# Kernel optimization log

Hardware: AMD Instinct MI355X
Metric: run time of the kernel (lower is better)

The kernel has to match this reference:

```python
import jax, jax.numpy as jnp
import numpy as np

D_MODEL = 1024
NHEAD = 16
HEAD_DIM = D_MODEL // NHEAD
D_FF = 4096
EPS = 1e-8


def rmsnorm(x, w):
    # matches torch: norm = ||x||_2 / sqrt(d); out = w * x / (rms + eps)
    rms = jnp.linalg.norm(x, axis=-1, keepdims=True) / np.sqrt(x.shape[-1])
    return w * (x / (rms + EPS))


def setup_inputs() -> dict:
    key = jax.random.key(0)
    ks = jax.random.split(key, 11)
    B, S = 4, 2048
    init = lambda k, shape, fan_in: jax.random.uniform(k, shape, jnp.float32, -1.0, 1.0) / np.sqrt(fan_in)
    return {
        "src": jax.random.normal(ks[0], (B, S, D_MODEL), jnp.float32),
        "qkv_w": init(ks[1], (D_MODEL, 3 * D_MODEL), D_MODEL),
        "qkv_b": init(ks[2], (3 * D_MODEL,), D_MODEL),
        "out_w": init(ks[3], (D_MODEL, D_MODEL), D_MODEL),
        "out_b": init(ks[4], (D_MODEL,), D_MODEL),
        "ff1_w": init(ks[5], (D_MODEL, D_FF), D_MODEL),
        "ff1_b": init(ks[6], (D_FF,), D_MODEL),
        "ff2_w": init(ks[7], (D_FF, D_MODEL), D_FF),
        "ff2_b": init(ks[8], (D_MODEL,), D_FF),
        "norm1_w": jnp.ones((D_MODEL,), jnp.float32),
        "norm2_w": jnp.ones((D_MODEL,), jnp.float32),
    }


def reference(src, qkv_w, qkv_b, out_w, out_b, ff1_w, ff1_b, ff2_w, ff2_b, norm1_w, norm2_w):
    B, S, _ = src.shape
    # --- pre-norm attention block ---
    x = rmsnorm(src, norm1_w)
    qkv = x @ qkv_w + qkv_b                     # [B,S,3*D]
    qkv = qkv.reshape(B, S, 3, NHEAD, HEAD_DIM)
    q, k, v = qkv[:, :, 0], qkv[:, :, 1], qkv[:, :, 2]   # [B,S,H,D]
    scores = jnp.einsum('bshd,bthd->bhst', q, k) / np.sqrt(HEAD_DIM)
    attn = jax.nn.softmax(scores, axis=-1)
    ctx = jnp.einsum('bhst,bthd->bshd', attn, v).reshape(B, S, D_MODEL)
    src = src + ctx @ out_w + out_b
    # --- pre-norm FFN block ---
    y = rmsnorm(src, norm2_w)
    h = jax.nn.gelu(y @ ff1_w + ff1_b, approximate=False)
    src = src + h @ ff2_w + ff2_b
    return src
```

## Files before the change

### kernel.cpp

```cpp
#include <hip/hip_runtime.h>
#include <hip/hip_bf16.h>

#define DM   1024
#define DFF  4096
#define NH   16
#define HD   64
#define SEQ  2048
#define BATCH 4
#define NTOK (BATCH*SEQ)

typedef float  f32x4  __attribute__((ext_vector_type(4)));
typedef short  bf16x8 __attribute__((ext_vector_type(8)));

#define SBAR() asm volatile("s_barrier" ::: "memory")
#define S_VMCNT(N) asm volatile("s_waitcnt vmcnt(" #N ")" ::: "memory")

__device__ __forceinline__ unsigned short f2bf(float f) {
    unsigned int x = __builtin_bit_cast(unsigned int, f);
    x += 0x7fff + ((x >> 16) & 1);
    return (unsigned short)(x >> 16);
}
__device__ __forceinline__ float bf2f(unsigned short u) {
    unsigned int x = (unsigned int)u << 16;
    return __builtin_bit_cast(float, x);
}

__device__ __forceinline__ float fexp2(float x) {
    float r; asm("v_exp_f32 %0, %1" : "=v"(r) : "v"(x)); return r;
}
__device__ __forceinline__ float frcp(float x) {
    float r; asm("v_rcp_f32 %0, %1" : "=v"(r) : "v"(x)); return r;
}

__device__ __forceinline__ void gload_lds16(const void* g, void* l) {
    __builtin_amdgcn_global_load_lds(
        (const __attribute__((address_space(1))) unsigned int*)g,
        (__attribute__((address_space(3))) unsigned int*)l,
        16, 0, 0);
}

__device__ __forceinline__ int swz(int row, int elem) { return elem ^ ((row & 7) << 3); }

__global__ __launch_bounds__(256)
void prep_all(const float* __restrict__ qkv_w, const float* __restrict__ out_w,
              const float* __restrict__ ff1_w, const float* __restrict__ ff2_w,
              unsigned short* __restrict__ qkv_wt, unsigned short* __restrict__ out_wt,
              unsigned short* __restrict__ ff1_wt, unsigned short* __restrict__ ff2_wt,
              const float* __restrict__ src, const float* __restrict__ n1_w,
              unsigned short* __restrict__ xb)
{
    __shared__ float tile[32][33];
    int b = blockIdx.x;
    if (b < 12288) {
        const float* W; unsigned short* Wt; int K, N, bx, by;
        if (b < 3072)      { W = qkv_w; Wt = qkv_wt; K = 1024; N = 3072; bx = b % 96;  by = b / 96;  }
        else if (b < 4096) { int i = b - 3072; W = out_w; Wt = out_wt; K = 1024; N = 1024; bx = i % 32;  by = i / 32; }
        else if (b < 8192) { int i = b - 4096; W = ff1_w; Wt = ff1_wt; K = 1024; N = 4096; bx = i % 128; by = i / 128; }
        else               { int i = b - 8192; W = ff2_w; Wt = ff2_wt; K = 4096; N = 1024; bx = i % 32;  by = i / 32; }
        int n0 = bx * 32, k0 = by * 32;
        int tx = threadIdx.x & 31, ty = threadIdx.x >> 5;
        #pragma unroll
        for (int i = 0; i < 4; ++i)
            tile[ty + i*8][tx] = W[(size_t)(k0 + ty + i*8) * N + n0 + tx];
        __syncthreads();
        #pragma unroll
        for (int i = 0; i < 4; ++i)
            Wt[(size_t)(n0 + ty + i*8) * K + k0 + tx] = f2bf(tile[tx][ty + i*8]);
    } else {
        int row = b - 12288, t = threadIdx.x;
        float4 v = ((const float4*)(src + (size_t)row * DM))[t];
        float ss = v.x*v.x + v.y*v.y + v.z*v.z + v.w*v.w;
        #pragma unroll
        for (int m = 1; m < 64; m <<= 1) ss += __shfl_xor(ss, m);
        if ((t & 63) == 0) tile[0][t >> 6] = ss;
        __syncthreads();
        float tot = tile[0][0] + tile[0][1] + tile[0][2] + tile[0][3];
        float rms = sqrtf(tot) * (1.f / 32.f);
        float inv = 1.f / (rms + 1e-8f);
        float4 wv = ((const float4*)n1_w)[t];
        unsigned int lo = (unsigned int)f2bf(v.x*inv*wv.x) | ((unsigned int)f2bf(v.y*inv*wv.y) << 16);
        unsigned int hi = (unsigned int)f2bf(v.z*inv*wv.z) | ((unsigned int)f2bf(v.w*inv*wv.w) << 16);
        uint2 pk; pk.x = lo; pk.y = hi;
        *(uint2*)(xb + (size_t)row * DM + t * 4) = pk;
    }
}

__global__ __launch_bounds__(256)
void rmsnorm_kernel(const unsigned short* __restrict__ inp, const float* __restrict__ w,
                    unsigned short* __restrict__ out)
{
    __shared__ float red[4];
    int row = blockIdx.x, t = threadIdx.x;
    ushort4 u = ((const ushort4*)(inp + (size_t)row * DM))[t];
    float x0 = bf2f(u.x), x1 = bf2f(u.y), x2 = bf2f(u.z), x3 = bf2f(u.w);
    float ss = x0*x0 + x1*x1 + x2*x2 + x3*x3;
    #pragma unroll
    for (int m = 1; m < 64; m <<= 1) ss += __shfl_xor(ss, m);
    if ((t & 63) == 0) red[t >> 6] = ss;
    __syncthreads();
    float tot = red[0] + red[1] + red[2] + red[3];
    float rms = sqrtf(tot) * (1.f / 32.f);
    float inv = 1.f / (rms + 1e-8f);
    float4 wv = ((const float4*)w)[t];
    unsigned int lo = (unsigned int)f2bf(x0*inv*wv.x) | ((unsigned int)f2bf(x1*inv*wv.y) << 16);
    unsigned int hi = (unsigned int)f2bf(x2*inv*wv.z) | ((unsigned int)f2bf(x3*inv*wv.w) << 16);
    uint2 pk; pk.x = lo; pk.y = hi;
    *(uint2*)(out + (size_t)row * DM + t * 4) = pk;
}

template<int MODE, int NB>
__global__ __launch_bounds__(512, 2)
void gemm_tpl(const unsigned short* __restrict__ A,
              const unsigned short* __restrict__ Bt,
              const float* __restrict__ bias,
              int N, int K, int nx,
              const float* __restrict__ residf,
              const unsigned short* __restrict__ residb,
              float* __restrict__ outf,
              unsigned short* __restrict__ outb,
              unsigned short* __restrict__ q,
              unsigned short* __restrict__ kk,
              unsigned short* __restrict__ vt)
{
    constexpr int NJ = NB / 64;
    constexpr int WN = NB / 4;
    __shared__ __align__(16) unsigned short Atile[2][2][256 * 32];
    __shared__ __align__(16) unsigned short Btile[2][2][NB * 32];
    const int tid = threadIdx.x, w = tid >> 6, l = tid & 63;
    const int lr = l & 15, lh = l >> 4;
    const int wm = w >> 2, wn = w & 3;
    const int nwg = gridDim.x, cpx = nwg >> 3;
    const int sid = (blockIdx.x & 7) * cpx + (blockIdx.x >> 3);
    const int by = sid / nx, bx = sid - by * nx;
    const int m0 = by * 256, n0 = bx * NB;
    const int nkt = K >> 6;
    const int srow = w * 16 + (l >> 2);
    const int scol = (((l & 3) ^ (srow & 3)) << 3);

    auto stageA = [&](int kt, int ks, int half, int bi) {
        int r0 = half * 128;
        gload_lds16(A + (size_t)(m0 + r0 + srow) * K + kt * 64 + ks * 32 + scol,
                    &Atile[bi][ks][(r0 + w * 16) * 32]);
    };
    auto stageB = [&](int kt, int ks, int half, int bi) {
        int r0 = half * 128;
        gload_lds16(Bt + (size_t)(n0 + r0 + srow) * K + kt * 64 + ks * 32 + scol,
                    &Btile[bi][ks][(r0 + w * 16) * 32]);
    };

    f32x4 acc[8][NJ];
    #pragma unroll
    for (int a = 0; a < 8; ++a)
        #pragma unroll
        for (int j = 0; j < NJ; ++j) acc[a][j] = {0.f, 0.f, 0.f, 0.f};

    #pragma unroll
    for (int ks = 0; ks < 2; ++ks) {
        stageA(0, ks, 0, 0); stageA(0, ks, 1, 0);
        stageB(0, ks, 0, 0);
        if (NB == 256) stageB(0, ks, 1, 0);
    }

    int bi = 0;
    for (int t = 0; t < nkt; ++t) {
        #pragma unroll
        for (int ks = 0; ks < 2; ++ks) {
            if (ks == 0 || t + 1 < nkt) {
                if constexpr (NB == 256) { S_VMCNT(4); } else { S_VMCNT(3); }
            } else {
                S_VMCNT(0);
            }
            SBAR();
            bf16x8 bB[NJ];
            #pragma unroll
            for (int j = 0; j < NJ; ++j) {
                int row = wn * WN + j * 16 + lr;
                bB[j] = *(const bf16x8*)&Btile[bi][ks][row * 32 + ((lh ^ (row & 3)) << 3)];
            }
            #pragma unroll
            for (int rho = 0; rho < 2; ++rho) {
                bf16x8 aA[4];
                #pragma unroll
                for (int i = 0; i < 4; ++i) {
                    int row = wm * 128 + rho * 64 + i * 16 + lr;
                    aA[i] = *(const bf16x8*)&Atile[bi][ks][row * 32 + ((lh ^ (row & 3)) << 3)];
                }
                if (t + 1 < nkt) {
                    if (rho == 0) { stageA(t + 1, ks, 0, bi ^ 1); stageA(t + 1, ks, 1, bi ^ 1); }
                    else          { stageB(t + 1, ks, 0, bi ^ 1);
                                    if (NB == 256) stageB(t + 1, ks, 1, bi ^ 1); }
                }
                SBAR();
                __builtin_amdgcn_s_setprio(1);
                #pragma unroll
                for (int i = 0; i < 4; ++i)
                    #pragma unroll
                    for (int j = 0; j < NJ; ++j)
                        acc[rho * 4 + i][j] = __builtin_amdgcn_mfma_f32_16x16x32_bf16(
                            aA[i], bB[j], acc[rho * 4 + i][j], 0, 0, 0);
                __builtin_amdgcn_s_setprio(0);
            }
        }
        bi ^= 1;
    }

    #pragma unroll
    for (int a = 0; a < 8; ++a) {
        const int rho = a >> 2, i = a & 3;
        #pragma unroll
        for (int j = 0; j < NJ; ++j) {
            const int col = n0 + wn * WN + j * 16 + lr;
            const int row0 = m0 + wm * 128 + rho * 64 + i * 16 + lh * 4;
            if (MODE == 0) {
                float v0 = acc[a][j][0] + bias[col];
                float v1 = acc[a][j][1] + bias[col];
                float v2 = acc[a][j][2] + bias[col];
                float v3 = acc[a][j][3] + bias[col];
                int wh = col >> 10, h = (col >> 6) & 15, d = col & 63;
                int b = row0 >> 11, s0 = row0 & 2047;
                size_t base = (size_t)(b * NH + h);
                if (wh == 0) {
                    q[(base * SEQ + s0    ) * HD + d] = f2bf(v0 * 0.18033688f);
                    q[(base * SEQ + s0 + 1) * HD + d] = f2bf(v1 * 0.18033688f);
                    q[(base * SEQ + s0 + 2) * HD + d] = f2bf(v2 * 0.18033688f);
                    q[(base * SEQ + s0 + 3) * HD + d] = f2bf(v3 * 0.18033688f);
                } else if (wh == 1) {
                    kk[(base * SEQ + s0    ) * HD + d] = f2bf(v0);
                    kk[(base * SEQ + s0 + 1) * HD + d] = f2bf(v1);
                    kk[(base * SEQ + s0 + 2) * HD + d] = f2bf(v2);
                    kk[(base * SEQ + s0 + 3) * HD + d] = f2bf(v3);
                } else {
                    uint2 pk;
                    pk.x = (unsigned int)f2bf(v0) | ((unsigned int)f2bf(v1) << 16);
                    pk.y = (unsigned int)f2bf(v2) | ((unsigned int)f2bf(v3) << 16);
                    *(uint2*)&vt[(base * HD + d) * SEQ + s0] = pk;
                }
            } else {
                #pragma unroll
                for (int r = 0; r < 4; ++r) {
                    int row = row0 + r;
                    float v = acc[a][j][r] + bias[col];
                    if (MODE == 2) {
                        float x = v;
                        float t2 = fmaf(x * x * x, 0.044715f, x);
                        float av = fminf(t2 * 2.3022079f, 80.f);
                        float u = fexp2(av);
                        float g = x * u * frcp(u + 1.f);
                        outb[(size_t)row * N + col] = f2bf(g);
                    } else if (MODE == 3) {
                        outf[(size_t)row * N + col] = v + bf2f(residb[(size_t)row * N + col]);
                    } else {
                        outb[(size_t)row * N + col] = f2bf(v + residf[(size_t)row * N + col]);
                    }
                }
            }
        }
    }
}

__global__ __launch_bounds__(256, 2)
void attn_kernel(const unsigned short* __restrict__ q,
                 const unsigned short* __restrict__ k,
                 const unsigned short* __restrict__ vt,
                 unsigned short* __restrict__ ctx)
{
    __shared__ __align__(16) unsigned short Ks[2][64 * 64];
    __shared__ __align__(16) unsigned short Vs[2][64 * 64];
    __shared__ __align__(16) unsigned short PQ[4][64 * 64];

    const int tid = threadIdx.x, w = tid >> 6, l = tid & 63;
    const int lr = l & 15, lh = l >> 4;

    const int sid = (blockIdx.x & 7) * 64 + (blockIdx.x >> 3);
    const int bh = sid >> 3, qt = sid & 7;
    const int b = bh >> 4, h = bh & 15;

    const int rloc = l >> 3;
    const int cswz = (((l & 7) ^ rloc) << 3);

    const unsigned short* kbase0 = k  + (size_t)bh * SEQ * HD;
    const unsigned short* vbase0 = vt + (size_t)bh * HD * SEQ;
    const int NT = SEQ / 64;

    auto stageK = [&](int t, int buf) {
        const unsigned short* kb = kbase0 + (size_t)t * 64 * HD;
        #pragma unroll
        for (int c = 0; c < 2; ++c) {
            int r0 = (w * 2 + c) * 8;
            gload_lds16(kb + (size_t)(r0 + rloc) * HD + cswz, &Ks[buf][r0 * 64]);
        }
    };
    auto stageV = [&](int t, int buf) {
        const unsigned short* vb = vbase0 + t * 64;
        #pragma unroll
        for (int c = 0; c < 2; ++c) {
            int d0 = w * 16 + c * 8;
            gload_lds16(vb + (size_t)(d0 + rloc) * SEQ + cswz, &Vs[buf][d0 * 64]);
        }
    };

    unsigned short* Pw = &PQ[w][0];
    const unsigned short* qbase = q + ((size_t)bh * SEQ + qt * 256 + w * 64) * HD;
    #pragma unroll
    for (int c = 0; c < 8; ++c) {
        int r0 = c * 8;
        gload_lds16(qbase + (size_t)(r0 + rloc) * HD + cswz, &Pw[r0 * 64]);
    }
    stageK(0, 0);
    stageV(0, 0);
    S_VMCNT(4);
    bf16x8 aq[4][2];
    #pragma unroll
    for (int g = 0; g < 4; ++g) {
        int row = g * 16 + lr;
        aq[g][0] = *(const bf16x8*)&Pw[row * 64 + swz(row,      lh * 8)];
        aq[g][1] = *(const bf16x8*)&Pw[row * 64 + swz(row, 32 + lh * 8)];
    }
    __syncthreads();

    bf16x8 vone;
    #pragma unroll
    for (int i = 0; i < 8; ++i) vone[i] = (short)0x3F80;

    f32x4 lacc[4];
    f32x4 o[4][4];
    #pragma unroll
    for (int g = 0; g < 4; ++g) {
        lacc[g] = {0.f, 0.f, 0.f, 0.f};
        #pragma unroll
        for (int nf = 0; nf < 4; ++nf) o[g][nf] = {0.f, 0.f, 0.f, 0.f};
    }

    for (int t = 0; t < NT; ++t) {
        const int cur = t & 1;
        if (t + 1 < NT) { stageK(t + 1, cur ^ 1); stageV(t + 1, cur ^ 1); }

        const unsigned short* Kc = &Ks[cur][0];
        const unsigned short* Vc = &Vs[cur][0];

        bf16x8 kb[4][2];
        #pragma unroll
        for (int j = 0; j < 4; ++j) {
            int kr = j * 16 + lr;
            kb[j][0] = *(const bf16x8*)&Kc[kr * 64 + swz(kr,      lh * 8)];
            kb[j][1] = *(const bf16x8*)&Kc[kr * 64 + swz(kr, 32 + lh * 8)];
        }

        #pragma unroll
        for (int g = 0; g < 4; ++g) {
            f32x4 sc[4];
            __builtin_amdgcn_s_setprio(1);
            #pragma unroll
            for (int j = 0; j < 4; ++j) {
                f32x4 z = {0.f, 0.f, 0.f, 0.f};
                z = __builtin_amdgcn_mfma_f32_16x16x32_bf16(kb[j][0], aq[g][0], z, 0, 0, 0);
                z = __builtin_amdgcn_mfma_f32_16x16x32_bf16(kb[j][1], aq[g][1], z, 0, 0, 0);
                sc[j] = z;
            }
            __builtin_amdgcn_s_setprio(0);

            int prow = g * 16 + lr;
            #pragma unroll
            for (int j = 0; j < 4; ++j) {
                float p0 = fexp2(sc[j][0]), p1 = fexp2(sc[j][1]);
                float p2 = fexp2(sc[j][2]), p3 = fexp2(sc[j][3]);
                unsigned int w0, w1;
                asm("v_cvt_pk_bf16_f32 %0, %1, %2" : "=v"(w0) : "v"(p0), "v"(p1));
                asm("v_cvt_pk_bf16_f32 %0, %1, %2" : "=v"(w1) : "v"(p2), "v"(p3));
                int k0 = j * 16 + lh * 4;
                int e = prow * 64 + (k0 ^ ((prow & 7) << 3));
                uint2 pk; pk.x = w0; pk.y = w1;
                *(uint2*)&Pw[e] = pk;
            }
        }

        bf16x8 ap[4][2];
        #pragma unroll
        for (int g = 0; g < 4; ++g) {
            int prow = g * 16 + lr;
            ap[g][0] = *(const bf16x8*)&Pw[prow * 64 + swz(prow,      lh * 8)];
            ap[g][1] = *(const bf16x8*)&Pw[prow * 64 + swz(prow, 32 + lh * 8)];
        }
        __builtin_amdgcn_s_setprio(1);
        #pragma unroll
        for (int g = 0; g < 4; ++g) {
            lacc[g] = __builtin_amdgcn_mfma_f32_16x16x32_bf16(ap[g][0], vone, lacc[g], 0, 0, 0);
            lacc[g] = __builtin_amdgcn_mfma_f32_16x16x32_bf16(ap[g][1], vone, lacc[g], 0, 0, 0);
        }
        #pragma unroll
        for (int nf = 0; nf < 4; ++nf) {
            int vr = nf * 16 + lr;
            bf16x8 vb0 = *(const bf16x8*)&Vc[vr * 64 + swz(vr,      lh * 8)];
            bf16x8 vb1 = *(const bf16x8*)&Vc[vr * 64 + swz(vr, 32 + lh * 8)];
            #pragma unroll
            for (int g = 0; g < 4; ++g) {
                o[g][nf] = __builtin_amdgcn_mfma_f32_16x16x32_bf16(ap[g][0], vb0, o[g][nf], 0, 0, 0);
                o[g][nf] = __builtin_amdgcn_mfma_f32_16x16x32_bf16(ap[g][1], vb1, o[g][nf], 0, 0, 0);
            }
        }
        __builtin_amdgcn_s_setprio(0);

        __syncthreads();
    }

    #pragma unroll
    for (int g = 0; g < 4; ++g) {
        float linv[4];
        #pragma unroll
        for (int r = 0; r < 4; ++r) linv[r] = frcp(lacc[g][r]);
        #pragma unroll
        for (int nf = 0; nf < 4; ++nf)
            #pragma unroll
            for (int r = 0; r < 4; ++r) {
                int row = qt * 256 + w * 64 + g * 16 + lh * 4 + r;
                ctx[((size_t)b * SEQ + row) * DM + h * 64 + nf * 16 + lr] =
                    f2bf(o[g][nf][r] * linv[r]);
            }
    }
}

extern "C" void kernel_launch(void* const* d_in, const int* in_sizes, int n_in,
                              void* d_out, int out_size, void* d_ws, size_t ws_size,
                              hipStream_t stream)
{
    const float* src   = (const float*)d_in[0];
    const float* qkv_w = (const float*)d_in[1];
    const float* qkv_b = (const float*)d_in[2];
    const float* out_w = (const float*)d_in[3];
    const float* out_b = (const float*)d_in[4];
    const float* ff1_w = (const float*)d_in[5];
    const float* ff1_b = (const float*)d_in[6];
    const float* ff2_w = (const float*)d_in[7];
    const float* ff2_b = (const float*)d_in[8];
    const float* n1_w  = (const float*)d_in[9];
    const float* n2_w  = (const float*)d_in[10];

    char* ws = (char*)d_ws;
    const size_t MB = 1u << 20;
    unsigned short* qkv_wt = (unsigned short*)(ws);
    unsigned short* out_wt = (unsigned short*)(ws + 6*MB);
    unsigned short* ff1_wt = (unsigned short*)(ws + 8*MB);
    unsigned short* ff2_wt = (unsigned short*)(ws + 16*MB);
    unsigned short* xb     = (unsigned short*)(ws + 24*MB);
    unsigned short* qb     = (unsigned short*)(ws + 40*MB);
    unsigned short* kb     = (unsigned short*)(ws + 56*MB);
    unsigned short* vtb    = (unsigned short*)(ws + 72*MB);
    unsigned short* hb     = (unsigned short*)(ws + 24*MB);
    unsigned short* ctxb   = (unsigned short*)(ws + 88*MB);
    unsigned short* yb     = (unsigned short*)(ws + 88*MB);
    unsigned short* src2b  = (unsigned short*)(ws + 104*MB);
    float* outp = (float*)d_out;

    prep_all<<<12288 + NTOK, 256, 0, stream>>>(qkv_w, out_w, ff1_w, ff2_w,
                                               qkv_wt, out_wt, ff1_wt, ff2_wt,
                                               src, n1_w, xb);

    gemm_tpl<0, 256><<<384, 512, 0, stream>>>(xb, qkv_wt, qkv_b, 3072, 1024, 12,
                                              nullptr, nullptr, nullptr, nullptr, qb, kb, vtb);

    attn_kernel<<<SEQ/256 * BATCH*NH, 256, 0, stream>>>(qb, kb, vtb, ctxb);

    gemm_tpl<4, 128><<<256, 512, 0, stream>>>(ctxb, out_wt, out_b, 1024, 1024, 8,
                                              src, nullptr, nullptr, src2b, nullptr, nullptr, nullptr);

    rmsnorm_kernel<<<NTOK, 256, 0, stream>>>(src2b, n2_w, yb);

    gemm_tpl<2, 256><<<512, 512, 0, stream>>>(yb, ff1_wt, ff1_b, 4096, 1024, 16,
                                              nullptr, nullptr, nullptr, hb, nullptr, nullptr, nullptr);

    gemm_tpl<3, 128><<<256, 512, 0, stream>>>(hb, ff2_wt, ff2_b, 1024, 4096, 8,
                                              nullptr, src2b, outp, nullptr, nullptr, nullptr, nullptr);
}
```

Baseline: 378.1 us.

## Vectorize weight transpose and use N-major block order for FF2 GEMM

The weight-prep transpose now reads each 32x32 tile with one float4 load per thread and writes four packed bf16 values per thread, replacing four scalar loads and stores. The FF2 GEMM gets an N-major block ordering option, so each XCD group of consecutive blocks walks M tiles for a fixed N column. This aims to improve L2 reuse of the large K=4096 weight slab rather than the activation rows. The transpose's column reads from shared memory may now hit bank conflicts.

```diff
diff --git a/kernel.cpp b/kernel.cpp
--- a/kernel.cpp
+++ b/kernel.cpp
@@ -58,14 +58,21 @@
         else if (b < 8192) { int i = b - 4096; W = ff1_w; Wt = ff1_wt; K = 1024; N = 4096; bx = i % 128; by = i / 128; }
         else               { int i = b - 8192; W = ff2_w; Wt = ff2_wt; K = 4096; N = 1024; bx = i % 32;  by = i / 32; }
         int n0 = bx * 32, k0 = by * 32;
-        int tx = threadIdx.x & 31, ty = threadIdx.x >> 5;
-        #pragma unroll
-        for (int i = 0; i < 4; ++i)
-            tile[ty + i*8][tx] = W[(size_t)(k0 + ty + i*8) * N + n0 + tx];
+        int t = threadIdx.x;
+        {
+            int kr = t >> 3, nc = (t & 7) * 4;
+            float4 v = *(const float4*)&W[(size_t)(k0 + kr) * N + n0 + nc];
+            tile[kr][nc + 0] = v.x; tile[kr][nc + 1] = v.y;
+            tile[kr][nc + 2] = v.z; tile[kr][nc + 3] = v.w;
+        }
         __syncthreads();
-        #pragma unroll
-        for (int i = 0; i < 4; ++i)
-            Wt[(size_t)(n0 + ty + i*8) * K + k0 + tx] = f2bf(tile[tx][ty + i*8]);
+        {
+            int nr = t >> 3, kc = (t & 7) * 4;
+            uint2 pk;
+            pk.x = (unsigned int)f2bf(tile[kc + 0][nr]) | ((unsigned int)f2bf(tile[kc + 1][nr]) << 16);
+            pk.y = (unsigned int)f2bf(tile[kc + 2][nr]) | ((unsigned int)f2bf(tile[kc + 3][nr]) << 16);
+            *(uint2*)&Wt[(size_t)(n0 + nr) * K + k0 + kc] = pk;
+        }
     } else {
         int row = b - 12288, t = threadIdx.x;
         float4 v = ((const float4*)(src + (size_t)row * DM))[t];
@@ -108,12 +115,12 @@
     *(uint2*)(out + (size_t)row * DM + t * 4) = pk;
 }
 
-template<int MODE, int NB>
+template<int MODE, int NB, bool NMAJOR = false>
 __global__ __launch_bounds__(512, 2)
 void gemm_tpl(const unsigned short* __restrict__ A,
               const unsigned short* __restrict__ Bt,
               const float* __restrict__ bias,
-              int N, int K, int nx,
+              int N, int K, int nd,
               const float* __restrict__ residf,
               const unsigned short* __restrict__ residb,
               float* __restrict__ outf,
@@ -131,7 +138,9 @@
     const int wm = w >> 2, wn = w & 3;
     const int nwg = gridDim.x, cpx = nwg >> 3;
     const int sid = (blockIdx.x & 7) * cpx + (blockIdx.x >> 3);
-    const int by = sid / nx, bx = sid - by * nx;
+    int by, bx;
+    if constexpr (NMAJOR) { bx = sid / nd; by = sid - bx * nd; }
+    else                  { by = sid / nd; bx = sid - by * nd; }
     const int m0 = by * 256, n0 = bx * NB;
     const int nkt = K >> 6;
     const int srow = w * 16 + (l >> 2);
@@ -468,6 +477,6 @@
     gemm_tpl<2, 256><<<512, 512, 0, stream>>>(yb, ff1_wt, ff1_b, 4096, 1024, 16,
                                               nullptr, nullptr, nullptr, hb, nullptr, nullptr, nullptr);
 
-    gemm_tpl<3, 128><<<256, 512, 0, stream>>>(hb, ff2_wt, ff2_b, 1024, 4096, 8,
-                                              nullptr, src2b, outp, nullptr, nullptr, nullptr, nullptr);
-}
+    gemm_tpl<3, 128, true><<<256, 512, 0, stream>>>(hb, ff2_wt, ff2_b, 1024, 4096, 32,
+                                                    nullptr, src2b, outp, nullptr, nullptr, nullptr, nullptr);
+}
```

Result: slower. 399.1 us (+5.5%).
